# Kernel tuning notes

Hardware: AMD Instinct MI355X
Metric: run time of the kernel (lower is better)

Reference implementation:

```python
import jax, jax.numpy as jnp
import numpy as np

EPS = 1e-5

def layer_norm(x, w):
    mu = x.mean(-1, keepdims=True)
    var = x.var(-1, keepdims=True)
    return (x - mu) * jax.lax.rsqrt(var + EPS) * w

def multihead_norm(x, w):
    # x: (B,S,NH,DH) -> group norm per head, elementwise weight over NH*DH features
    mu = x.mean(-1, keepdims=True)
    var = x.var(-1, keepdims=True)
    xn = (x - mu) * jax.lax.rsqrt(var + EPS)
    B, S, NH, DH = x.shape
    return xn.reshape(B, S, NH * DH) * w

def causal_conv1d(x, W, b):
    # x: (B,S,C), W: (C,K) depthwise causal conv, bias b: (C,)
    C, K = W.shape
    ker = W.T[:, None, :]  # (K,1,C) in WIO layout
    y = jax.lax.conv_general_dilated(x, ker, (1,), [(K - 1, 0)],
                                     dimension_numbers=('NWC', 'WIO', 'NWC'),
                                     feature_group_count=C)
    return y + b

def headwise_linear(x, W):
    # block-diagonal linear; W: (nblocks, out, in)
    nb, o, i = W.shape
    B, S, F = x.shape
    y = jnp.einsum('bsni,noi->bsno', x.reshape(B, S, nb, i), W)
    return y.reshape(B, S, nb * o)

def mlstm_block(x, ln_w, up_W, conv_W, conv_b, q_W, k_W, v_W, ig_W, ig_b, fg_W, fg_b, on_w, skip, down_W):
    B, S, E = x.shape
    I = up_W.shape[1] // 2
    NH = ig_W.shape[0]
    DH = I // NH
    xn = layer_norm(x, ln_w)
    up = xn @ up_W                       # (B,S,2I)
    xm, z = up[..., :I], up[..., I:]
    xc = jax.nn.silu(causal_conv1d(xm, conv_W, conv_b))
    q = headwise_linear(xc, q_W)
    k = headwise_linear(xc, k_W)
    v = headwise_linear(xm, v_W)        # values come from the pre-conv branch
    gin = jnp.concatenate([q, k, v], -1)  # (B,S,3I)
    ig = (gin @ ig_W.T + ig_b).transpose(0, 2, 1)  # (B,NH,S)
    fg = (gin @ fg_W.T + fg_b).transpose(0, 2, 1)
    qh = q.reshape(B, S, NH, DH).transpose(0, 2, 1, 3)
    kh = k.reshape(B, S, NH, DH).transpose(0, 2, 1, 3)
    vh = v.reshape(B, S, NH, DH).transpose(0, 2, 1, 3)
    # parallel stabilized mLSTM (matrix memory)
    logf = jax.nn.log_sigmoid(fg)
    cs = jnp.concatenate([jnp.zeros_like(logf[..., :1]), jnp.cumsum(logf, -1)], -1)  # (B,NH,S+1)
    lf = cs[..., 1:, None] - cs[..., None, 1:]   # (B,NH,S,S): sum of log f over (t, s]
    mask = jnp.tril(jnp.ones((S, S), bool))
    log_D = jnp.where(mask, lf + ig[:, :, None, :], -jnp.inf)
    max_log_D = log_D.max(-1, keepdims=True)
    D = jnp.exp(log_D - max_log_D)
    qk = jnp.einsum('bhsd,bhtd->bhst', qh, kh) * (DH ** -0.5)
    C = qk * D
    normalizer = jnp.maximum(jnp.abs(C.sum(-1, keepdims=True)), jnp.exp(-max_log_D))
    h = jnp.einsum('bhst,bhtd->bhsd', C / (normalizer + 1e-6), vh)
    h = multihead_norm(h.transpose(0, 2, 1, 3), on_w)  # (B,S,I)
    h = (h + skip * xc) * jax.nn.silu(z)
    return x + h @ down_W

def slstm_block(x, ln_w, conv_W, conv_b, gates_W, R, bias, gn_w, ffn_ln_w, ffn_up_W, ffn_down_W):
    B, S, E = x.shape
    NH, DH = R.shape[0], R.shape[1]
    xn = layer_norm(x, ln_w)
    xc = jax.nn.silu(causal_conv1d(xn, conv_W, conv_b))
    xh = xn.reshape(B, S, NH, DH)
    xch = xc.reshape(B, S, NH, DH)
    i_pre = jnp.einsum('bsnd,nod->bsno', xch, gates_W[0])  # i,f gates see conv branch
    f_pre = jnp.einsum('bsnd,nod->bsno', xch, gates_W[1])
    z_pre = jnp.einsum('bsnd,nod->bsno', xh, gates_W[2])
    o_pre = jnp.einsum('bsnd,nod->bsno', xh, gates_W[3])
    gx = jnp.stack([i_pre, f_pre, z_pre, o_pre], 3) + bias  # (B,S,NH,4,DH)
    def step(carry, g):
        h, c, n, m = carry
        raw = g + jnp.einsum('bnd,ndg->bng', h, R).reshape(B, NH, 4, DH)
        ir, fr, zr, og = raw[:, :, 0], raw[:, :, 1], raw[:, :, 2], raw[:, :, 3]
        logfplusm = m + jax.nn.log_sigmoid(fr)
        m_new = jnp.maximum(ir, logfplusm)
        i = jnp.exp(ir - m_new)
        f = jnp.exp(logfplusm - m_new)
        c_new = f * c + i * jnp.tanh(zr)
        n_new = f * n + i
        h_new = jax.nn.sigmoid(og) * c_new / n_new
        return (h_new, c_new, n_new, m_new), h_new
    z0 = jnp.zeros((B, NH, DH), x.dtype)
    _, hs = jax.lax.scan(step, (z0, z0, z0, z0), gx.transpose(1, 0, 2, 3, 4))
    y = multihead_norm(hs.transpose(1, 0, 2, 3), gn_w)  # (B,S,E)
    x = x + y
    xn2 = layer_norm(x, ffn_ln_w)
    gpre, upp = jnp.split(xn2 @ ffn_up_W, 2, -1)
    return x + (jax.nn.gelu(gpre, approximate=False) * upp) @ ffn_down_W

def forward(x, m_ln_w, m_up_W, m_conv_W, m_conv_b, m_q_W, m_k_W, m_v_W, m_ig_W, m_ig_b, m_fg_W, m_fg_b, m_outnorm_w, m_skip, m_down_W, s_ln_w, s_conv_W, s_conv_b, s_gates_W, s_R, s_bias, s_gn_w, s_ffn_ln_w, s_ffn_up_W, s_ffn_down_W, post_norm_w, fc_W, fc_b):
    mi = 0
    for blk in range(7):  # slstm_at=[1]
        if blk == 1:
            x = slstm_block(x, s_ln_w, s_conv_W, s_conv_b, s_gates_W, s_R, s_bias, s_gn_w, s_ffn_ln_w, s_ffn_up_W, s_ffn_down_W)
        else:
            x = mlstm_block(x, m_ln_w[mi], m_up_W[mi], m_conv_W[mi], m_conv_b[mi], m_q_W[mi], m_k_W[mi], m_v_W[mi], m_ig_W[mi], m_ig_b[mi], m_fg_W[mi], m_fg_b[mi], m_outnorm_w[mi], m_skip[mi], m_down_W[mi])
            mi += 1
    x = layer_norm(x, post_norm_w)
    return x[:, -1, :] @ fc_W + fc_b

def setup_inputs():
    key = jax.random.key(0)
    ks = jax.random.split(key, 18)
    B, S, E = 16, 512, 128
    I, NH = 256, 4
    DHs = E // NH
    FF = 192
    NB = 6
    r = lambda k, shape, sc: jax.random.normal(k, shape, jnp.float32) * sc
    return dict(
        x=r(ks[0], (B, S, E), 1.0),
        m_ln_w=jnp.ones((NB, E), jnp.float32),
        m_up_W=r(ks[1], (NB, E, 2 * I), E ** -0.5),
        m_conv_W=r(ks[2], (NB, I, 4), 0.3),
        m_conv_b=jnp.zeros((NB, I), jnp.float32),
        m_q_W=r(ks[3], (NB, 64, 4, 4), 0.5),
        m_k_W=r(ks[4], (NB, 64, 4, 4), 0.5),
        m_v_W=r(ks[5], (NB, 64, 4, 4), 0.5),
        m_ig_W=r(ks[6], (NB, NH, 3 * I), 0.1 * (3 * I) ** -0.5),
        m_ig_b=r(ks[7], (NB, NH), 0.5),
        m_fg_W=r(ks[8], (NB, NH, 3 * I), 0.1 * (3 * I) ** -0.5),
        m_fg_b=r(ks[9], (NB, NH), 1.0) + 3.0,
        m_outnorm_w=jnp.ones((NB, I), jnp.float32),
        m_skip=jnp.ones((NB, I), jnp.float32),
        m_down_W=r(ks[10], (NB, I, E), I ** -0.5),
        s_ln_w=jnp.ones((E,), jnp.float32),
        s_conv_W=r(ks[11], (E, 4), 0.3),
        s_conv_b=jnp.zeros((E,), jnp.float32),
        s_gates_W=r(ks[12], (4, NH, DHs, DHs), DHs ** -0.5),
        s_R=r(ks[13], (NH, DHs, 4 * DHs), 0.5 * DHs ** -0.5),
        s_bias=r(ks[14], (NH, 4, DHs), 0.1),
        s_gn_w=jnp.ones((E,), jnp.float32),
        s_ffn_ln_w=jnp.ones((E,), jnp.float32),
        s_ffn_up_W=r(ks[15], (E, 2 * FF), E ** -0.5),
        s_ffn_down_W=r(ks[16], (FF, E), FF ** -0.5),
        post_norm_w=jnp.ones((E,), jnp.float32),
        fc_W=r(ks[17], (E, 1), E ** -0.5),
        fc_b=jnp.zeros((1,), jnp.float32),
    )

def reference(x, m_ln_w, m_up_W, m_conv_W, m_conv_b, m_q_W, m_k_W, m_v_W, m_ig_W, m_ig_b, m_fg_W, m_fg_b, m_outnorm_w, m_skip, m_down_W, s_ln_w, s_conv_W, s_conv_b, s_gates_W, s_R, s_bias, s_gn_w, s_ffn_ln_w, s_ffn_up_W, s_ffn_down_W, post_norm_w, fc_W, fc_b):
    return forward(x, m_ln_w, m_up_W, m_conv_W, m_conv_b, m_q_W, m_k_W, m_v_W, m_ig_W, m_ig_b, m_fg_W, m_fg_b, m_outnorm_w, m_skip, m_down_W, s_ln_w, s_conv_W, s_conv_b, s_gates_W, s_R, s_bias, s_gn_w, s_ffn_ln_w, s_ffn_up_W, s_ffn_down_W, post_norm_w, fc_W, fc_b)
```

## Files before the change

kernel.cpp:

```cpp
#include <hip/hip_runtime.h>
#include <cstddef>

constexpr int B = 16, S = 512, E = 128, I = 256, DHm = 64;
constexpr int BS = B * S;

typedef _Float16 half8 __attribute__((ext_vector_type(8)));
typedef _Float16 half4 __attribute__((ext_vector_type(4)));
typedef float f32x4 __attribute__((ext_vector_type(4)));

__device__ __forceinline__ int swz(int row, int col) {
  return (row * 64 + col) ^ ((row & 7) << 3);
}
struct h3s { _Float16 a, b, c; };
__device__ __forceinline__ h3s split3(float x) {
  h3s r;
  r.a = (_Float16)x;
  float t = x - (float)r.a;
  r.b = (_Float16)t;
  t -= (float)r.b;
  r.c = (_Float16)t;
  return r;
}
struct h2s { _Float16 a, b; };
__device__ __forceinline__ h2s split2(float x) {
  h2s r;
  r.a = (_Float16)x;
  r.b = (_Float16)(x - (float)r.a);
  return r;
}

template <int K, bool ADD, int FUSE>
__global__ void __launch_bounds__(256) gemm3(const float* __restrict__ A,
                                             const float* __restrict__ W,
                                             const float* __restrict__ lnw,
                                             float* __restrict__ C, int N, int astride) {
  __shared__ _Float16 A1[4096], A2[4096];
  __shared__ _Float16 B1[4096], B2[4096];
  __shared__ float smu[64], srr[64];
  const int n0 = blockIdx.x * 64, m0 = blockIdx.y * 64;
  const int tid = threadIdx.x;
  const int lane = tid & 63, w = tid >> 6;
  const int sband = w * 16;
  const int fr = lane & 15, fg = lane >> 4;

  if constexpr (FUSE == 1) {
    int row = tid >> 2, q = tid & 3;
    const float* ap = A + (size_t)(m0 + row) * astride + q * 32;
    float s1 = 0.f, s2 = 0.f;
#pragma unroll
    for (int i = 0; i < 8; i++) {
      float4 v = *(const float4*)(ap + i * 4);
      s1 += v.x + v.y + v.z + v.w;
      s2 += v.x * v.x + v.y * v.y + v.z * v.z + v.w * v.w;
    }
    s1 += __shfl_xor(s1, 1); s2 += __shfl_xor(s2, 1);
    s1 += __shfl_xor(s1, 2); s2 += __shfl_xor(s2, 2);
    if (q == 0) {
      float mu = s1 * (1.f / 128);
      float var = s2 * (1.f / 128) - mu * mu;
      smu[row] = mu;
      srr[row] = rsqrtf(var + 1e-5f);
    }
  }

  f32x4 acc[4] = {};
#pragma unroll
  for (int k0 = 0; k0 < K; k0 += 64) {
    __syncthreads();
#pragma unroll
    for (int i = 0; i < 4; i++) {
      int lin = tid + i * 256;
      int mm = lin >> 4, kq = (lin & 15) * 4;
      float4 a4;
      if constexpr (FUSE == 2) {
// ... 27 lines not shown
    }
#pragma unroll
    for (int i = 0; i < 4; i++) {
      int lin = tid + i * 256;
      int kk = lin >> 4, nq = (lin & 15) * 4;
      float4 w4 = *(const float4*)(W + (size_t)(k0 + kk) * N + n0 + nq);
      const float wv[4] = {w4.x, w4.y, w4.z, w4.w};
#pragma unroll
      for (int j = 0; j < 4; j++) {
        h2s sp = split2(wv[j]);
        B1[swz(nq + j, kk)] = sp.a;
        B2[swz(nq + j, kk)] = sp.b;
      }
    }
    __syncthreads();
    half8 a1g0 = *(const half8*)&A1[swz(sband + fr, fg * 8)];
    half8 a1g1 = *(const half8*)&A1[swz(sband + fr, 32 + fg * 8)];
    half8 a2g0 = *(const half8*)&A2[swz(sband + fr, fg * 8)];
    half8 a2g1 = *(const half8*)&A2[swz(sband + fr, 32 + fg * 8)];
#pragma unroll
    for (int ct = 0; ct < 4; ct++) {
      half8 b1g0 = *(const half8*)&B1[swz(ct * 16 + fr, fg * 8)];
      half8 b1g1 = *(const half8*)&B1[swz(ct * 16 + fr, 32 + fg * 8)];
      half8 b2g0 = *(const half8*)&B2[swz(ct * 16 + fr, fg * 8)];
      half8 b2g1 = *(const half8*)&B2[swz(ct * 16 + fr, 32 + fg * 8)];
      acc[ct] = __builtin_amdgcn_mfma_f32_16x16x32_f16(a2g0, b1g0, acc[ct], 0, 0, 0);
      acc[ct] = __builtin_amdgcn_mfma_f32_16x16x32_f16(a1g0, b2g0, acc[ct], 0, 0, 0);
      acc[ct] = __builtin_amdgcn_mfma_f32_16x16x32_f16(a1g0, b1g0, acc[ct], 0, 0, 0);
      acc[ct] = __builtin_amdgcn_mfma_f32_16x16x32_f16(a2g1, b1g1, acc[ct], 0, 0, 0);
      acc[ct] = __builtin_amdgcn_mfma_f32_16x16x32_f16(a1g1, b2g1, acc[ct], 0, 0, 0);
      acc[ct] = __builtin_amdgcn_mfma_f32_16x16x32_f16(a1g1, b1g1, acc[ct], 0, 0, 0);
    }
  }
#pragma unroll
  for (int ct = 0; ct < 4; ct++) {
#pragma unroll
    for (int r = 0; r < 4; r++) {
      int row = m0 + sband + fg * 4 + r;
      int col = n0 + ct * 16 + fr;
      float v = acc[ct][r];
      if (ADD) v += C[(size_t)row * N + col];
      C[(size_t)row * N + col] = v;
    }
  }
}

__global__ void __launch_bounds__(256) mlstm_mid_kernel(
    const float* __restrict__ UP, const float* __restrict__ conv_W,
    const float* __restrict__ conv_b, const float* __restrict__ qW,
    const float* __restrict__ kW, const float* __restrict__ vW,
    const float* __restrict__ igW, const float* __restrict__ igb,
    const float* __restrict__ fgW, const float* __restrict__ fgb,
    float* __restrict__ XC, float* __restrict__ Q,
    _Float16* __restrict__ K1, _Float16* __restrict__ K2, _Float16* __restrict__ K3,
    _Float16* __restrict__ V1t, _Float16* __restrict__ V2t, _Float16* __restrict__ V3t,
    float* __restrict__ IG, float* __restrict__ FG) {
  __shared__ float xcl[I], xml[I], qkvl[768];
  __shared__ float red[32];
  int r = blockIdx.x, t = threadIdx.x;
  int s = r & (S - 1);
  const float* xr = UP + (size_t)r * 512 + t;
  float4 w4 = *(const float4*)(conv_W + t * 4);
  float x0 = xr[0];
  float acc = conv_b[t] + x0 * w4.w;
  if (s >= 1) acc += xr[-512] * w4.z;
  if (s >= 2) acc += xr[-1024] * w4.y;
  if (s >= 3) acc += xr[-1536] * w4.x;
  float xc = acc / (1.f + __expf(-acc));
  xcl[t] = xc;
  xml[t] = x0;
  XC[(size_t)r * I + t] = xc;
  __syncthreads();
  int n = t >> 2, o = t & 3;
  const float* qw = qW + n * 16 + o * 4;
  const float* kw = kW + n * 16 + o * 4;
  const float* vw = vW + n * 16 + o * 4;
  float q = 0, k = 0, v = 0;
#pragma unroll
  for (int i = 0; i < 4; i++) {
    float xcv = xcl[n * 4 + i], xmv = xml[n * 4 + i];
    q += xcv * qw[i]; k += xcv * kw[i]; v += xmv * vw[i];
  }
  Q[(size_t)r * I + t] = q;
  {
    h3s sp = split3(k);
    K1[(size_t)r * I + t] = sp.a;
    K2[(size_t)r * I + t] = sp.b;
    K3[(size_t)r * I + t] = sp.c;
  }
  {
    int b = r >> 9, srow = r & (S - 1);
    int h = t >> 6, d = t & 63;
    size_t idx = ((size_t)(b * 4 + h) * 64 + d) * S + srow;
    h3s sp = split3(v);
    V1t[idx] = sp.a;
    V2t[idx] = sp.b;
    V3t[idx] = sp.c;
  }
  qkvl[t] = q; qkvl[256 + t] = k; qkvl[512 + t] = v;
  __syncthreads();
  float ai[4] = {}, af[4] = {};
#pragma unroll
  for (int j = 0; j < 3; j++) {
    int c = t + j * 256;
    float g = qkvl[c];
#pragma unroll
    for (int h = 0; h < 4; h++) {
      ai[h] += g * igW[h * 768 + c];
      af[h] += g * fgW[h * 768 + c];
    }
  }
#pragma unroll
  for (int m = 32; m; m >>= 1)
#pragma unroll
    for (int h = 0; h < 4; h++) {
      ai[h] += __shfl_xor(ai[h], m);
      af[h] += __shfl_xor(af[h], m);
    }
  int wv = t >> 6;
  if ((t & 63) == 0) {
#pragma unroll
    for (int h = 0; h < 4; h++) { red[wv * 8 + h] = ai[h]; red[wv * 8 + 4 + h] = af[h]; }
  }
  __syncthreads();
  if (t < 8) {
    float sum = red[t] + red[8 + t] + red[16 + t] + red[24 + t];
    int b = r >> 9, srow = r & (S - 1);
    int h = t & 3;
    if (t < 4) IG[((size_t)(b * 4 + h)) * S + srow] = sum + igb[h];
    else FG[((size_t)(b * 4 + h)) * S + srow] = sum + fgb[h];
  }
}

__global__ void __launch_bounds__(256) attn_mfma_kernel(
    const float* __restrict__ Q,
    const _Float16* __restrict__ K1g, const _Float16* __restrict__ K2g,
    const _Float16* __restrict__ K3g, const _Float16* __restrict__ V1g,
    const _Float16* __restrict__ V2g, const _Float16* __restrict__ V3g,
    const float* __restrict__ IG, const float* __restrict__ FG,
    const float* __restrict__ XC, const float* __restrict__ UP,
    const float* __restrict__ onw, const float* __restrict__ skip,
    float* __restrict__ HF) {
  __shared__ _Float16 K1[4096], K2[4096], K3[4096];
  __shared__ _Float16 V1[4096], V2[4096], V3[4096];
  __shared__ _Float16 W1[4096], W2[4096], W3[4096];
  __shared__ float A_l[512], M_l[512], F_l[512];
  int bid = blockIdx.x;
  int st = bid & 7, bh = bid >> 3;
  int b = bh >> 2, h = bh & 3;
  int s0 = st * 64;
  int tid = threadIdx.x;
  const float* Qg = Q + ((size_t)b * S) * I + h * DHm;
  const _Float16* K1p = K1g + ((size_t)b * S) * I + h * DHm;
  const _Float16* K2p = K2g + ((size_t)b * S) * I + h * DHm;
  const _Float16* K3p = K3g + ((size_t)b * S) * I + h * DHm;
  const _Float16* V1p = V1g + (size_t)bh * 64 * S;
  const _Float16* V2p = V2g + (size_t)bh * 64 * S;
  const _Float16* V3p = V3g + (size_t)bh * 64 * S;

  const int lane = tid & 63, w = tid >> 6;
  const int sband = w * 16;
  const int fr = lane & 15, fg = lane >> 4;

  if (tid < 64) {
    int l = tid;
    const float* ig = IG + (size_t)bh * S;
    const float* fgp = FG + (size_t)bh * S;
    float lfc[8], av[8], amx[8];
    float cs = 0;
#pragma unroll
    for (int j = 0; j < 8; j++) {
      float f = fgp[l * 8 + j];
      cs += fminf(f, 0.f) - log1pf(__expf(-fabsf(f)));
      lfc[j] = cs;
    }
    float tot = cs, inc = tot;
#pragma unroll
    for (int off = 1; off < 64; off <<= 1) {
      float yv = __shfl_up(inc, off);
      if (l >= off) inc += yv;
    }
    float excl = inc - tot;
    float pm = -1e30f;
#pragma unroll
    for (int j = 0; j < 8; j++) {
      float CSj = excl + lfc[j];
      av[j] = ig[l * 8 + j] - CSj;
      pm = fmaxf(pm, av[j]);
      amx[j] = pm;
      lfc[j] = CSj;
    }
    float incm = pm;
#pragma unroll
    for (int off = 1; off < 64; off <<= 1) {
      float yv = __shfl_up(incm, off);
      if (l >= off) incm = fmaxf(incm, yv);
    }
    float exclm = __shfl_up(incm, 1);
    if (l == 0) exclm = -1e30f;
#pragma unroll
    for (int j = 0; j < 8; j++) {
      float Mj = fmaxf(exclm, amx[j]);
      A_l[l * 8 + j] = av[j];
      M_l[l * 8 + j] = Mj;
      F_l[l * 8 + j] = __expf(-(lfc[j] + Mj));
    }
  }

  half8 aq1[2], aq2[2], aq3[2];
  {
    const float* qrow = Qg + (size_t)(s0 + sband + fr) * I;
#pragma unroll
    for (int c = 0; c < 2; c++) {
      float4 qa = *(const float4*)(qrow + c * 32 + fg * 8);
      float4 qb = *(const float4*)(qrow + c * 32 + fg * 8 + 4);
      float qv[8] = {qa.x, qa.y, qa.z, qa.w, qb.x, qb.y, qb.z, qb.w};
#pragma unroll
      for (int j = 0; j < 8; j++) {
        h3s sp = split3(qv[j]);
        aq1[c][j] = sp.a; aq2[c][j] = sp.b; aq3[c][j] = sp.c;
      }
    }
  }
  __syncthreads();
  float msl[4];
#pragma unroll
  for (int r = 0; r < 4; r++) msl[r] = M_l[s0 + sband + fg * 4 + r];

  f32x4 hacc[4] = {};
  float csp[4] = {};

  for (int tt = 0; tt <= st; tt++) {
    int t0 = tt * 64;
    __syncthreads();
#pragma unroll
    for (int i = 0; i < 4; i++) {
      int lin = tid + i * 256;
      int a = lin >> 4, q4 = (lin & 15) * 4;
      size_t koff = (size_t)(t0 + a) * I + q4;
      *(half4*)&K1[swz(a, q4)] = *(const half4*)(K1p + koff);
      *(half4*)&K2[swz(a, q4)] = *(const half4*)(K2p + koff);
      *(half4*)&K3[swz(a, q4)] = *(const half4*)(K3p + koff);
      size_t voff = (size_t)a * S + t0 + q4;
      *(half4*)&V1[swz(a, q4)] = *(const half4*)(V1p + voff);
      *(half4*)&V2[swz(a, q4)] = *(const half4*)(V2p + voff);
      *(half4*)&V3[swz(a, q4)] = *(const half4*)(V3p + voff);
    }
    __syncthreads();
#pragma unroll
    for (int ct = 0; ct < 4; ct++) {
      f32x4 sacc = {};
#pragma unroll
      for (int c = 0; c < 2; c++) {
        half8 b1 = *(const half8*)&K1[swz(ct * 16 + fr, c * 32 + fg * 8)];
        half8 b2 = *(const half8*)&K2[swz(ct * 16 + fr, c * 32 + fg * 8)];
        half8 b3 = *(const half8*)&K3[swz(ct * 16 + fr, c * 32 + fg * 8)];
        sacc = __builtin_amdgcn_mfma_f32_16x16x32_f16(aq3[c], b1, sacc, 0, 0, 0);
        sacc = __builtin_amdgcn_mfma_f32_16x16x32_f16(aq2[c], b2, sacc, 0, 0, 0);
        sacc = __builtin_amdgcn_mfma_f32_16x16x32_f16(aq1[c], b3, sacc, 0, 0, 0);
        sacc = __builtin_amdgcn_mfma_f32_16x16x32_f16(aq2[c], b1, sacc, 0, 0, 0);
        sacc = __builtin_amdgcn_mfma_f32_16x16x32_f16(aq1[c], b2, sacc, 0, 0, 0);
        sacc = __builtin_amdgcn_mfma_f32_16x16x32_f16(aq1[c], b1, sacc, 0, 0, 0);
      }
      int tg = t0 + ct * 16 + fr;
      float ea = A_l[tg];
#pragma unroll
      for (int r = 0; r < 4; r++) {
        int sl = sband + fg * 4 + r;
        float wv = 0.f;
        if (tg <= s0 + sl) wv = sacc[r] * 0.125f * __expf(ea - msl[r]);
        csp[r] += wv;
        h3s sp = split3(wv);
        W1[swz(sl, ct * 16 + fr)] = sp.a;
        W2[swz(sl, ct * 16 + fr)] = sp.b;
        W3[swz(sl, ct * 16 + fr)] = sp.c;
      }
    }
#pragma unroll
    for (int kc = 0; kc < 2; kc++) {
      half8 w1 = *(const half8*)&W1[swz(sband + fr, kc * 32 + fg * 8)];
      half8 w2 = *(const half8*)&W2[swz(sband + fr, kc * 32 + fg * 8)];
      half8 w3 = *(const half8*)&W3[swz(sband + fr, kc * 32 + fg * 8)];
#pragma unroll
      for (int dt = 0; dt < 4; dt++) {
        half8 v1 = *(const half8*)&V1[swz(dt * 16 + fr, kc * 32 + fg * 8)];
        half8 v2 = *(const half8*)&V2[swz(dt * 16 + fr, kc * 32 + fg * 8)];
        half8 v3 = *(const half8*)&V3[swz(dt * 16 + fr, kc * 32 + fg * 8)];
        hacc[dt] = __builtin_amdgcn_mfma_f32_16x16x32_f16(w3, v1, hacc[dt], 0, 0, 0);
        hacc[dt] = __builtin_amdgcn_mfma_f32_16x16x32_f16(w2, v2, hacc[dt], 0, 0, 0);
        hacc[dt] = __builtin_amdgcn_mfma_f32_16x16x32_f16(w1, v3, hacc[dt], 0, 0, 0);
        hacc[dt] = __builtin_amdgcn_mfma_f32_16x16x32_f16(w2, v1, hacc[dt], 0, 0, 0);
        hacc[dt] = __builtin_amdgcn_mfma_f32_16x16x32_f16(w1, v2, hacc[dt], 0, 0, 0);
        hacc[dt] = __builtin_amdgcn_mfma_f32_16x16x32_f16(w1, v1, hacc[dt], 0, 0, 0);
      }
    }
  }
#pragma unroll
  for (int m = 1; m < 16; m <<= 1)
#pragma unroll
    for (int r = 0; r < 4; r++) csp[r] += __shfl_xor(csp[r], m);
  float on4[4], sk4[4];
#pragma unroll
  for (int dt = 0; dt < 4; dt++) {
    on4[dt] = onw[h * DHm + dt * 16 + fr];
    sk4[dt] = skip[h * DHm + dt * 16 + fr];
  }
#pragma unroll
  for (int r = 0; r < 4; r++) {
    int sl = sband + fg * 4 + r;
    size_t row = (size_t)b * S + s0 + sl;
    float Fv = F_l[s0 + sl];
    float inv = 1.f / (fmaxf(fabsf(csp[r]), Fv) + 1e-6f);
    float hv[4], s1 = 0.f, s2 = 0.f;
#pragma unroll
    for (int dt = 0; dt < 4; dt++) {
      hv[dt] = hacc[dt][r] * inv;
      s1 += hv[dt];
      s2 += hv[dt] * hv[dt];
    }
#pragma unroll
    for (int m = 1; m < 16; m <<= 1) { s1 += __shfl_xor(s1, m); s2 += __shfl_xor(s2, m); }
    float mu = s1 * (1.f / 64), var = s2 * (1.f / 64) - mu * mu;
    float rr = rsqrtf(var + 1e-5f);
#pragma unroll
    for (int dt = 0; dt < 4; dt++) {
      int col = h * DHm + dt * 16 + fr;
      float xc = XC[row * I + col];
      float zv = UP[row * (2 * I) + I + col];
      float hn = (hv[dt] - mu) * rr * on4[dt];
      HF[row * I + col] = (hn + sk4[dt] * xc) * (zv / (1.f + __expf(-zv)));
    }
  }
}

__global__ void __launch_bounds__(512) slstm_pre_kernel(
    const float* __restrict__ X, const float* __restrict__ lnw,
    const float* __restrict__ conv_W, const float* __restrict__ conv_b,
    const float* __restrict__ gW, const float* __restrict__ bias,
    float* __restrict__ GX) {
  __shared__ float xnl[4][128], xcl[128];
  __shared__ float redS[8], redQ[8];
  int r = blockIdx.x, t = threadIdx.x;
  int s = r & (S - 1);
  int b0 = r - s;
  int rr = t >> 7, cc = t & 127;
  int sr = s - 3 + rr;
  int grow = b0 + (sr > 0 ? sr : 0);
  float x = X[(size_t)grow * E + cc];
  float s1 = x, s2 = x * x;
#pragma unroll
  for (int m = 32; m; m >>= 1) { s1 += __shfl_xor(s1, m); s2 += __shfl_xor(s2, m); }
  int wv = t >> 6;
  if ((t & 63) == 0) { redS[wv] = s1; redQ[wv] = s2; }
  __syncthreads();
  float fs1 = redS[rr * 2] + redS[rr * 2 + 1];
  float fs2 = redQ[rr * 2] + redQ[rr * 2 + 1];
  float mu = fs1 * (1.f / 128);
  float var = fs2 * (1.f / 128) - mu * mu;
  xnl[rr][cc] = (x - mu) * rsqrtf(var + 1e-5f) * lnw[cc];
  __syncthreads();
  if (t < 128) {
    float4 w4 = *(const float4*)(conv_W + t * 4);
    float acc = conv_b[t] + xnl[3][t] * w4.w;
    if (s >= 1) acc += xnl[2][t] * w4.z;
    if (s >= 2) acc += xnl[1][t] * w4.y;
    if (s >= 3) acc += xnl[0][t] * w4.x;
    xcl[t] = acc / (1.f + __expf(-acc));
  }
  __syncthreads();
  int n = t >> 7, g = (t >> 5) & 3, o = t & 31;
  const float* src = (g < 2) ? (xcl + n * 32) : (xnl[3] + n * 32);
  const float* wp = gW + (((size_t)g * 4 + n) * 32 + o) * 32;
  float acc = bias[n * 128 + g * 32 + o];
#pragma unroll
  for (int d = 0; d < 32; d++) acc += src[d] * wp[d];
  GX[(size_t)r * 512 + t] = acc;
}

__global__ void __launch_bounds__(128) slstm_scan8(const float* __restrict__ GX,
                                                   const float* __restrict__ R,
                                                   float* __restrict__ HS) {
  constexpr int CH = 16, NCH = S / CH;
  __shared__ float ring[2][CH][128];
  int blk = blockIdx.x;
  int b = blk >> 2, n = blk & 3;
  int tid = threadIdx.x;
  int wv = tid >> 6, l = tid & 63;
  const float* gxp = GX + ((size_t)b * S) * 512 + n * 128;

  float R0[32], R1[32];
  float h_own = 0.f, c = 0.f, nn = 0.f, m = 0.f;
  if (wv == 0) {
#pragma unroll
    for (int d = 0; d < 32; d++) {
      R0[d] = R[((size_t)(n * 32 + d)) * 128 + l];
      R1[d] = R[((size_t)(n * 32 + d)) * 128 + 64 + l];
    }
  } else {
    float v0[CH], v1[CH];
#pragma unroll
    for (int j = 0; j < CH; j++) {
      v0[j] = gxp[(size_t)j * 512 + l];
      v1[j] = gxp[(size_t)j * 512 + 64 + l];
    }
#pragma unroll
    for (int j = 0; j < CH; j++) {
      ring[0][j][l] = v0[j];
      ring[0][j][64 + l] = v1[j];
    }
  }
  __syncthreads();

  for (int ck = 0; ck < NCH; ck++) {
    if (wv == 1) {
      if (ck + 1 < NCH) {
        const float* src = gxp + (size_t)(ck + 1) * CH * 512;
        float v0[CH], v1[CH];
#pragma unroll
        for (int j = 0; j < CH; j++) {
          v0[j] = src[(size_t)j * 512 + l];
          v1[j] = src[(size_t)j * 512 + 64 + l];
        }
        int pb = (ck + 1) & 1;
#pragma unroll
        for (int j = 0; j < CH; j++) {
          ring[pb][j][l] = v0[j];
          ring[pb][j][64 + l] = v1[j];
        }
      }
    } else {
      int cb = ck & 1;
#pragma unroll
      for (int j = 0; j < CH; j++) {
        float g0 = ring[cb][j][l];
        float g1 = ring[cb][j][64 + l];
        float r0p0 = g0, r0p1 = 0.f, r0p2 = 0.f, r0p3 = 0.f;
        float r1p0 = g1, r1p1 = 0.f, r1p2 = 0.f, r1p3 = 0.f;
#pragma unroll
        for (int d = 0; d < 32; d += 4) {
          float hv0 = __shfl(h_own, d);
          float hv1 = __shfl(h_own, d + 1);
          float hv2 = __shfl(h_own, d + 2);
          float hv3 = __shfl(h_own, d + 3);
          r0p0 += hv0 * R0[d];     r1p0 += hv0 * R1[d];
          r0p1 += hv1 * R0[d + 1]; r1p1 += hv1 * R1[d + 1];
          r0p2 += hv2 * R0[d + 2]; r1p2 += hv2 * R1[d + 2];
          r0p3 += hv3 * R0[d + 3]; r1p3 += hv3 * R1[d + 3];
        }
        float raw0 = (r0p0 + r0p1) + (r0p2 + r0p3);
        float raw1 = (r1p0 + r1p1) + (r1p2 + r1p3);
        float fr = __shfl_down(raw0, 32);
        float og = __shfl_down(raw1, 32);
        float ir = raw0, zr = raw1;
        float lsf = fminf(fr, 0.f) - __logf(1.f + __expf(-fabsf(fr)));
        float lfm = m + lsf;
        float mn = fmaxf(ir, lfm);
        float iv = __expf(ir - mn), fv = __expf(lfm - mn);
        float th = 1.f - 2.f / (__expf(2.f * zr) + 1.f);
        c = fv * c + iv * th;
        nn = fv * nn + iv;
        m = mn;
        float hv = (c / nn) / (1.f + __expf(-og));
        h_own = hv;
        int s = ck * CH + j;
        if (l < 32) HS[((size_t)(b * S + s)) * E + n * 32 + l] = hv;
      }
    }
    __syncthreads();
  }
}

__global__ void gnorm_add_kernel(const float* __restrict__ HS, const float* __restrict__ gnw,
                                 float* __restrict__ X) {
  int r = blockIdx.x, t = threadIdx.x;
  float v = HS[(size_t)r * E + t];
  float s1 = v, s2 = v * v;
#pragma unroll
  for (int m = 16; m; m >>= 1) { s1 += __shfl_xor(s1, m, 32); s2 += __shfl_xor(s2, m, 32); }
  float mu = s1 * (1.f / 32), var = s2 * (1.f / 32) - mu * mu;
  X[(size_t)r * E + t] += (v - mu) * rsqrtf(var + 1e-5f) * gnw[t];
}

__global__ void head_kernel(const float* __restrict__ X, const float* __restrict__ pw,
                            const float* __restrict__ fcW, const float* __restrict__ fcb,
                            float* __restrict__ out) {
  int b = blockIdx.x, l = threadIdx.x;
  const float* xr = X + ((size_t)(b * S + S - 1)) * E;
  float2 v = *(const float2*)(xr + l * 2);
  float s1 = v.x + v.y, s2 = v.x * v.x + v.y * v.y;
#pragma unroll
  for (int m = 32; m; m >>= 1) { s1 += __shfl_xor(s1, m); s2 += __shfl_xor(s2, m); }
  float mu = s1 * (1.f / E), var = s2 * (1.f / E) - mu * mu;
  float rr = rsqrtf(var + 1e-5f);
  float2 wv = *(const float2*)(pw + l * 2);
  float2 fw = *(const float2*)(fcW + l * 2);
  float acc = (v.x - mu) * rr * wv.x * fw.x + (v.y - mu) * rr * wv.y * fw.y;
#pragma unroll
  for (int m = 32; m; m >>= 1) acc += __shfl_xor(acc, m);
  if (l == 0) out[b] = acc + fcb[0];
}

extern "C" void kernel_launch(void* const* d_in, const int* in_sizes, int n_in, void* d_out,
                              int out_size, void* d_ws, size_t ws_size, hipStream_t stream) {
  const float* in_x = (const float*)d_in[0];
  const float* m_ln_w = (const float*)d_in[1];
  const float* m_up_W = (const float*)d_in[2];
  const float* m_conv_W = (const float*)d_in[3];
  const float* m_conv_b = (const float*)d_in[4];
  const float* m_q_W = (const float*)d_in[5];
  const float* m_k_W = (const float*)d_in[6];
  const float* m_v_W = (const float*)d_in[7];
  const float* m_ig_W = (const float*)d_in[8];
  const float* m_ig_b = (const float*)d_in[9];
  const float* m_fg_W = (const float*)d_in[10];
  const float* m_fg_b = (const float*)d_in[11];
  const float* m_on_w = (const float*)d_in[12];
  const float* m_skip = (const float*)d_in[13];
  const float* m_down_W = (const float*)d_in[14];
  const float* s_ln_w = (const float*)d_in[15];
  const float* s_conv_W = (const float*)d_in[16];
  const float* s_conv_b = (const float*)d_in[17];
  const float* s_gates_W = (const float*)d_in[18];
  const float* s_R = (const float*)d_in[19];
  const float* s_bias = (const float*)d_in[20];
  const float* s_gn_w = (const float*)d_in[21];
  const float* s_ffn_ln_w = (const float*)d_in[22];
  const float* s_ffn_up_W = (const float*)d_in[23];
  const float* s_ffn_down_W = (const float*)d_in[24];
  const float* post_norm_w = (const float*)d_in[25];
  const float* fc_W = (const float*)d_in[26];
  const float* fc_b = (const float*)d_in[27];

  float* ws = (float*)d_ws;
  float* X = ws;
  float* UP = X + 1048576;
  float* XC = UP + 4194304;
  float* Qb = XC + 2097152;
  float* Hb = Qb + 2097152;
  float* IGb = Hb + 2097152;
  float* FGb = IGb + 32768;
  _Float16* F16 = (_Float16*)(FGb + 32768);
  _Float16* K1 = F16;
  _Float16* K2 = K1 + 2097152;
  _Float16* K3 = K2 + 2097152;
  _Float16* V1t = K3 + 2097152;
  _Float16* V2t = V1t + 2097152;
  _Float16* V3t = V2t + 2097152;

  hipMemcpyAsync(X, in_x, (size_t)BS * E * sizeof(float), hipMemcpyDeviceToDevice, stream);

  int mi = 0;
  for (int blk = 0; blk < 7; blk++) {
    if (blk == 1) {
      slstm_pre_kernel<<<BS, 512, 0, stream>>>(X, s_ln_w, s_conv_W, s_conv_b, s_gates_W,
                                               s_bias, UP);
      slstm_scan8<<<64, 128, 0, stream>>>(UP, s_R, Hb);
      gnorm_add_kernel<<<BS, E, 0, stream>>>(Hb, s_gn_w, X);
      gemm3<128, false, 1><<<dim3(6, 128), 256, 0, stream>>>(X, s_ffn_up_W, s_ffn_ln_w, UP,
                                                             384, 128);
      gemm3<192, true, 2><<<dim3(2, 128), 256, 0, stream>>>(UP, s_ffn_down_W, nullptr, X,
                                                            128, 384);
    } else {
      const float* ln_w = m_ln_w + (size_t)mi * E;
      const float* up_W = m_up_W + (size_t)mi * E * 512;
      const float* conv_W = m_conv_W + (size_t)mi * I * 4;
      const float* conv_b = m_conv_b + (size_t)mi * I;
      const float* q_W = m_q_W + (size_t)mi * 1024;
      const float* k_W = m_k_W + (size_t)mi * 1024;
      const float* v_W = m_v_W + (size_t)mi * 1024;
      const float* ig_W = m_ig_W + (size_t)mi * 3072;
      const float* ig_b = m_ig_b + (size_t)mi * 4;
      const float* fg_W = m_fg_W + (size_t)mi * 3072;
      const float* fg_b = m_fg_b + (size_t)mi * 4;
      const float* on_w = m_on_w + (size_t)mi * I;
      const float* skipv = m_skip + (size_t)mi * I;
      const float* down_W = m_down_W + (size_t)mi * I * E;

      gemm3<128, false, 1><<<dim3(8, 128), 256, 0, stream>>>(X, up_W, ln_w, UP, 512, 128);
      mlstm_mid_kernel<<<BS, 256, 0, stream>>>(UP, conv_W, conv_b, q_W, k_W, v_W, ig_W, ig_b,
                                               fg_W, fg_b, XC, Qb, K1, K2, K3, V1t, V2t, V3t,
                                               IGb, FGb);
      attn_mfma_kernel<<<512, 256, 0, stream>>>(Qb, K1, K2, K3, V1t, V2t, V3t, IGb, FGb, XC,
                                                UP, on_w, skipv, Hb);
      gemm3<256, true, 0><<<dim3(2, 128), 256, 0, stream>>>(Hb, down_W, nullptr, X, 128, 256);
      mi++;
    }
  }
  head_kernel<<<B, 64, 0, stream>>>(X, post_norm_w, fc_W, fc_b, (float*)d_out);
}
```

Baseline: 1.279 ms.

## Pair causal query tiles per block to balance work and share K/V loads

Each attention block now handles two query tiles, a long one (7-st4) and a short one (st4), so every block runs the same number of key/value tile iterations under the causal mask. The grid shrinks from 512 to 256 blocks. K/V tiles staged in shared memory are reused by both query tiles, which removes duplicate global loads. In exchange each block holds twice as many accumulators and Q fragments, which raises register pressure and may lower occupancy.

Measured after the change: 1.311 ms. 2.6% more time.

```diff
diff --git a/kernel.cpp b/kernel.cpp
--- a/kernel.cpp
+++ b/kernel.cpp
@@ -247,9 +247,10 @@
   __shared__ _Float16 W1[4096], W2[4096], W3[4096];
   __shared__ float A_l[512], M_l[512], F_l[512];
   int bid = blockIdx.x;
-  int st = bid & 7, bh = bid >> 3;
+  int st4 = bid & 3, bh = bid >> 2;
   int b = bh >> 2, h = bh & 3;
-  int s0 = st * 64;
+  const int stA = 7 - st4, stB = st4;
+  const int s0A = stA * 64, s0B = stB * 64;
   int tid = threadIdx.x;
   const float* Qg = Q + ((size_t)b * S) * I + h * DHm;
   const _Float16* K1p = K1g + ((size_t)b * S) * I + h * DHm;
@@ -308,30 +309,42 @@
     }
   }
 
-  half8 aq1[2], aq2[2], aq3[2];
+  half8 aq1A[2], aq2A[2], aq3A[2], aq1B[2], aq2B[2], aq3B[2];
   {
-    const float* qrow = Qg + (size_t)(s0 + sband + fr) * I;
+    const float* qrowA = Qg + (size_t)(s0A + sband + fr) * I;
+    const float* qrowB = Qg + (size_t)(s0B + sband + fr) * I;
 #pragma unroll
     for (int c = 0; c < 2; c++) {
-      float4 qa = *(const float4*)(qrow + c * 32 + fg * 8);
-      float4 qb = *(const float4*)(qrow + c * 32 + fg * 8 + 4);
+      float4 qa = *(const float4*)(qrowA + c * 32 + fg * 8);
+      float4 qb = *(const float4*)(qrowA + c * 32 + fg * 8 + 4);
       float qv[8] = {qa.x, qa.y, qa.z, qa.w, qb.x, qb.y, qb.z, qb.w};
 #pragma unroll
       for (int j = 0; j < 8; j++) {
         h3s sp = split3(qv[j]);
-        aq1[c][j] = sp.a; aq2[c][j] = sp.b; aq3[c][j] = sp.c;
+        aq1A[c][j] = sp.a; aq2A[c][j] = sp.b; aq3A[c][j] = sp.c;
+      }
+      float4 qc = *(const float4*)(qrowB + c * 32 + fg * 8);
+      float4 qd = *(const float4*)(qrowB + c * 32 + fg * 8 + 4);
+      float qw[8] = {qc.x, qc.y, qc.z, qc.w, qd.x, qd.y, qd.z, qd.w};
+#pragma unroll
+      for (int j = 0; j < 8; j++) {
+        h3s sp = split3(qw[j]);
+        aq1B[c][j] = sp.a; aq2B[c][j] = sp.b; aq3B[c][j] = sp.c;
       }
     }
   }
   __syncthreads();
-  float msl[4];
-#pragma unroll
-  for (int r = 0; r < 4; r++) msl[r] = M_l[s0 + sband + fg * 4 + r];
-
-  f32x4 hacc[4] = {};
-  float csp[4] = {};
-
-  for (int tt = 0; tt <= st; tt++) {
+  float mslA[4], mslB[4];
+#pragma unroll
+  for (int r = 0; r < 4; r++) {
+    mslA[r] = M_l[s0A + sband + fg * 4 + r];
+    mslB[r] = M_l[s0B + sband + fg * 4 + r];
+  }
+
+  f32x4 haccA[4] = {}, haccB[4] = {};
+  float cspA[4] = {}, cspB[4] = {};
+
+  for (int tt = 0; tt <= stA; tt++) {
     int t0 = tt * 64;
     __syncthreads();
 #pragma unroll
@@ -356,12 +369,15 @@
         half8 b1 = *(const half8*)&K1[swz(ct * 16 + fr, c * 32 + fg * 8)];
         half8 b2 = *(const half8*)&K2[swz(ct * 16 + fr, c * 32 + fg * 8)];
         half8 b3 = *(const half8*)&K3[swz(ct * 16 + fr, c * 32 + fg * 8)];
-        sacc = __builtin_amdgcn_mfma_f32_16x16x32_f16(aq3[c], b1, sacc, 0, 0, 0);
-        sacc = __builtin_amdgcn_mfma_f32_16x16x32_f16(aq2[c], b2, sacc, 0, 0, 0);
-        sacc = __builtin_amdgcn_mfma_f32_16x16x32_f16(aq1[c], b3, sacc, 0, 0, 0);
-        sacc = __builtin_amdgcn_mfma_f32_16x16x32_f16(aq2[c], b1, sacc, 0, 0, 0);
-        sacc = __builtin_amdgcn_mfma_f32_16x16x32_f16(aq1[c], b2, sacc, 0, 0, 0);
-        sacc = __builtin_amdgcn_mfma_f32_16x16x32_f16(aq1[c], b1, sacc, 0, 0, 0);
+        half8 a1 = c ? aq1A[1] : aq1A[0];
+        half8 a2 = c ? aq2A[1] : aq2A[0];
+        half8 a3 = c ? aq3A[1] : aq3A[0];
+        sacc = __builtin_amdgcn_mfma_f32_16x16x32_f16(a3, b1, sacc, 0, 0, 0);
+        sacc = __builtin_amdgcn_mfma_f32_16x16x32_f16(a2, b2, sacc, 0, 0, 0);
+        sacc = __builtin_amdgcn_mfma_f32_16x16x32_f16(a1, b3, sacc, 0, 0, 0);
+        sacc = __builtin_amdgcn_mfma_f32_16x16x32_f16(a2, b1, sacc, 0, 0, 0);
+        sacc = __builtin_amdgcn_mfma_f32_16x16x32_f16(a1, b2, sacc, 0, 0, 0);
+        sacc = __builtin_amdgcn_mfma_f32_16x16x32_f16(a1, b1, sacc, 0, 0, 0);
       }
       int tg = t0 + ct * 16 + fr;
       float ea = A_l[tg];
@@ -369,8 +385,8 @@
       for (int r = 0; r < 4; r++) {
         int sl = sband + fg * 4 + r;
         float wv = 0.f;
-        if (tg <= s0 + sl) wv = sacc[r] * 0.125f * __expf(ea - msl[r]);
-        csp[r] += wv;
+        if (tg <= s0A + sl) wv = sacc[r] * 0.125f * __expf(ea - mslA[r]);
+        cspA[r] += wv;
         h3s sp = split3(wv);
         W1[swz(sl, ct * 16 + fr)] = sp.a;
         W2[swz(sl, ct * 16 + fr)] = sp.b;
@@ -387,19 +403,74 @@
         half8 v1 = *(const half8*)&V1[swz(dt * 16 + fr, kc * 32 + fg * 8)];
         half8 v2 = *(const half8*)&V2[swz(dt * 16 + fr, kc * 32 + fg * 8)];
         half8 v3 = *(const half8*)&V3[swz(dt * 16 + fr, kc * 32 + fg * 8)];
-        hacc[dt] = __builtin_amdgcn_mfma_f32_16x16x32_f16(w3, v1, hacc[dt], 0, 0, 0);
-        hacc[dt] = __builtin_amdgcn_mfma_f32_16x16x32_f16(w2, v2, hacc[dt], 0, 0, 0);
-        hacc[dt] = __builtin_amdgcn_mfma_f32_16x16x32_f16(w1, v3, hacc[dt], 0, 0, 0);
-        hacc[dt] = __builtin_amdgcn_mfma_f32_16x16x32_f16(w2, v1, hacc[dt], 0, 0, 0);
-        hacc[dt] = __builtin_amdgcn_mfma_f32_16x16x32_f16(w1, v2, hacc[dt], 0, 0, 0);
-        hacc[dt] = __builtin_amdgcn_mfma_f32_16x16x32_f16(w1, v1, hacc[dt], 0, 0, 0);
+        haccA[dt] = __builtin_amdgcn_mfma_f32_16x16x32_f16(w3, v1, haccA[dt], 0, 0, 0);
+        haccA[dt] = __builtin_amdgcn_mfma_f32_16x16x32_f16(w2, v2, haccA[dt], 0, 0, 0);
+        haccA[dt] = __builtin_amdgcn_mfma_f32_16x16x32_f16(w1, v3, haccA[dt], 0, 0, 0);
+        haccA[dt] = __builtin_amdgcn_mfma_f32_16x16x32_f16(w2, v1, haccA[dt], 0, 0, 0);
+        haccA[dt] = __builtin_amdgcn_mfma_f32_16x16x32_f16(w1, v2, haccA[dt], 0, 0, 0);
+        haccA[dt] = __builtin_amdgcn_mfma_f32_16x16x32_f16(w1, v1, haccA[dt], 0, 0, 0);
+      }
+    }
+    if (tt <= stB) {
+#pragma unroll
+      for (int ct = 0; ct < 4; ct++) {
+        f32x4 sacc = {};
+#pragma unroll
+        for (int c = 0; c < 2; c++) {
+          half8 b1 = *(const half8*)&K1[swz(ct * 16 + fr, c * 32 + fg * 8)];
+          half8 b2 = *(const half8*)&K2[swz(ct * 16 + fr, c * 32 + fg * 8)];
+          half8 b3 = *(const half8*)&K3[swz(ct * 16 + fr, c * 32 + fg * 8)];
+          half8 a1 = c ? aq1B[1] : aq1B[0];
+          half8 a2 = c ? aq2B[1] : aq2B[0];
+          half8 a3 = c ? aq3B[1] : aq3B[0];
+          sacc = __builtin_amdgcn_mfma_f32_16x16x32_f16(a3, b1, sacc, 0, 0, 0);
+          sacc = __builtin_amdgcn_mfma_f32_16x16x32_f16(a2, b2, sacc, 0, 0, 0);
+          sacc = __builtin_amdgcn_mfma_f32_16x16x32_f16(a1, b3, sacc, 0, 0, 0);
+          sacc = __builtin_amdgcn_mfma_f32_16x16x32_f16(a2, b1, sacc, 0, 0, 0);
+          sacc = __builtin_amdgcn_mfma_f32_16x16x32_f16(a1, b2, sacc, 0, 0, 0);
+          sacc = __builtin_amdgcn_mfma_f32_16x16x32_f16(a1, b1, sacc, 0, 0, 0);
+        }
+        int tg = t0 + ct * 16 + fr;
+        float ea = A_l[tg];
+#pragma unroll
+        for (int r = 0; r < 4; r++) {
+          int sl = sband + fg * 4 + r;
+          float wv = 0.f;
+          if (tg <= s0B + sl) wv = sacc[r] * 0.125f * __expf(ea - mslB[r]);
+          cspB[r] += wv;
+          h3s sp = split3(wv);
+          W1[swz(sl, ct * 16 + fr)] = sp.a;
+          W2[swz(sl, ct * 16 + fr)] = sp.b;
+          W3[swz(sl, ct * 16 + fr)] = sp.c;
+        }
+      }
+#pragma unroll
+      for (int kc = 0; kc < 2; kc++) {
+        half8 w1 = *(const half8*)&W1[swz(sband + fr, kc * 32 + fg * 8)];
+        half8 w2 = *(const half8*)&W2[swz(sband + fr, kc * 32 + fg * 8)];
+        half8 w3 = *(const half8*)&W3[swz(sband + fr, kc * 32 + fg * 8)];
+#pragma unroll
+        for (int dt = 0; dt < 4; dt++) {
+          half8 v1 = *(const half8*)&V1[swz(dt * 16 + fr, kc * 32 + fg * 8)];
+          half8 v2 = *(const half8*)&V2[swz(dt * 16 + fr, kc * 32 + fg * 8)];
+          half8 v3 = *(const half8*)&V3[swz(dt * 16 + fr, kc * 32 + fg * 8)];
+          haccB[dt] = __builtin_amdgcn_mfma_f32_16x16x32_f16(w3, v1, haccB[dt], 0, 0, 0);
+          haccB[dt] = __builtin_amdgcn_mfma_f32_16x16x32_f16(w2, v2, haccB[dt], 0, 0, 0);
+          haccB[dt] = __builtin_amdgcn_mfma_f32_16x16x32_f16(w1, v3, haccB[dt], 0, 0, 0);
+          haccB[dt] = __builtin_amdgcn_mfma_f32_16x16x32_f16(w2, v1, haccB[dt], 0, 0, 0);
+          haccB[dt] = __builtin_amdgcn_mfma_f32_16x16x32_f16(w1, v2, haccB[dt], 0, 0, 0);
+          haccB[dt] = __builtin_amdgcn_mfma_f32_16x16x32_f16(w1, v1, haccB[dt], 0, 0, 0);
+        }
       }
     }
   }
 #pragma unroll
   for (int m = 1; m < 16; m <<= 1)
 #pragma unroll
-    for (int r = 0; r < 4; r++) csp[r] += __shfl_xor(csp[r], m);
+    for (int r = 0; r < 4; r++) {
+      cspA[r] += __shfl_xor(cspA[r], m);
+      cspB[r] += __shfl_xor(cspB[r], m);
+    }
   float on4[4], sk4[4];
 #pragma unroll
   for (int dt = 0; dt < 4; dt++) {
@@ -407,29 +478,34 @@
     sk4[dt] = skip[h * DHm + dt * 16 + fr];
   }
 #pragma unroll
-  for (int r = 0; r < 4; r++) {
-    int sl = sband + fg * 4 + r;
-    size_t row = (size_t)b * S + s0 + sl;
-    float Fv = F_l[s0 + sl];
-    float inv = 1.f / (fmaxf(fabsf(csp[r]), Fv) + 1e-6f);
-    float hv[4], s1 = 0.f, s2 = 0.f;
-#pragma unroll
-    for (int dt = 0; dt < 4; dt++) {
-      hv[dt] = hacc[dt][r] * inv;
-      s1 += hv[dt];
-      s2 += hv[dt] * hv[dt];
-    }
-#pragma unroll
-    for (int m = 1; m < 16; m <<= 1) { s1 += __shfl_xor(s1, m); s2 += __shfl_xor(s2, m); }
-    float mu = s1 * (1.f / 64), var = s2 * (1.f / 64) - mu * mu;
-    float rr = rsqrtf(var + 1e-5f);
-#pragma unroll
-    for (int dt = 0; dt < 4; dt++) {
-      int col = h * DHm + dt * 16 + fr;
-      float xc = XC[row * I + col];
-      float zv = UP[row * (2 * I) + I + col];
-      float hn = (hv[dt] - mu) * rr * on4[dt];
-      HF[row * I + col] = (hn + sk4[dt] * xc) * (zv / (1.f + __expf(-zv)));
+  for (int part = 0; part < 2; part++) {
+    int s0p = part ? s0B : s0A;
+#pragma unroll
+    for (int r = 0; r < 4; r++) {
+      int sl = sband + fg * 4 + r;
+      size_t row = (size_t)b * S + s0p + sl;
+      float Fv = F_l[s0p + sl];
+      float cspv = part ? cspB[r] : cspA[r];
+      float inv = 1.f / (fmaxf(fabsf(cspv), Fv) + 1e-6f);
+      float hv[4], s1 = 0.f, s2 = 0.f;
+#pragma unroll
+      for (int dt = 0; dt < 4; dt++) {
+        hv[dt] = (part ? haccB[dt][r] : haccA[dt][r]) * inv;
+        s1 += hv[dt];
+        s2 += hv[dt] * hv[dt];
+      }
+#pragma unroll
+      for (int m = 1; m < 16; m <<= 1) { s1 += __shfl_xor(s1, m); s2 += __shfl_xor(s2, m); }
+      float mu = s1 * (1.f / 64), var = s2 * (1.f / 64) - mu * mu;
+      float rr = rsqrtf(var + 1e-5f);
+#pragma unroll
+      for (int dt = 0; dt < 4; dt++) {
+        int col = h * DHm + dt * 16 + fr;
+        float xc = XC[row * I + col];
+        float zv = UP[row * (2 * I) + I + col];
+        float hn = (hv[dt] - mu) * rr * on4[dt];
+        HF[row * I + col] = (hn + sk4[dt] * xc) * (zv / (1.f + __expf(-zv)));
+      }
     }
   }
 }
@@ -681,7 +757,7 @@
       mlstm_mid_kernel<<<BS, 256, 0, stream>>>(UP, conv_W, conv_b, q_W, k_W, v_W, ig_W, ig_b,
                                                fg_W, fg_b, XC, Qb, K1, K2, K3, V1t, V2t, V3t,
                                                IGb, FGb);
-      attn_mfma_kernel<<<512, 256, 0, stream>>>(Qb, K1, K2, K3, V1t, V2t, V3t, IGb, FGb, XC,
+      attn_mfma_kernel<<<256, 256, 0, stream>>>(Qb, K1, K2, K3, V1t, V2t, V3t, IGb, FGb, XC,
                                                 UP, on_w, skipv, Hb);
       gemm3<256, true, 0><<<dim3(2, 128), 256, 0, stream>>>(Hb, down_W, nullptr, X, 128, 256);
       mi++;
```

## Use two-term fp16 splits in mLSTM attention and fuse sLSTM groupnorm into scan

Applied to the files above, without the earlier changes.

The mLSTM attention used to emulate fp32 matmuls with a three-way fp16 split and six MFMAs per product. It now uses a two-way split with three MFMAs, which removes the K3/V3/W3 buffers, their global and LDS traffic, and half the MFMA work. The sLSTM per-head group norm and residual add are also folded into the scan kernel, so one launch and the HS round trip go away. The lower-precision split risks accuracy loss in the attention products.

Measured after the change: 1.098 ms. -14.1%, faster.

```diff
diff --git a/kernel.cpp b/kernel.cpp
--- a/kernel.cpp
+++ b/kernel.cpp
@@ -10,16 +10,6 @@
 
 __device__ __forceinline__ int swz(int row, int col) {
   return (row * 64 + col) ^ ((row & 7) << 3);
-}
-struct h3s { _Float16 a, b, c; };
-__device__ __forceinline__ h3s split3(float x) {
-  h3s r;
-  r.a = (_Float16)x;
-  float t = x - (float)r.a;
-  r.b = (_Float16)t;
-  t -= (float)r.b;
-  r.c = (_Float16)t;
-  return r;
 }
 struct h2s { _Float16 a, b; };
 __device__ __forceinline__ h2s split2(float x) {
@@ -153,8 +143,8 @@
     const float* __restrict__ igW, const float* __restrict__ igb,
     const float* __restrict__ fgW, const float* __restrict__ fgb,
     float* __restrict__ XC, float* __restrict__ Q,
-    _Float16* __restrict__ K1, _Float16* __restrict__ K2, _Float16* __restrict__ K3,
-    _Float16* __restrict__ V1t, _Float16* __restrict__ V2t, _Float16* __restrict__ V3t,
+    _Float16* __restrict__ K1, _Float16* __restrict__ K2,
+    _Float16* __restrict__ V1t, _Float16* __restrict__ V2t,
     float* __restrict__ IG, float* __restrict__ FG) {
   __shared__ float xcl[I], xml[I], qkvl[768];
   __shared__ float red[32];
@@ -184,19 +174,17 @@
   }
   Q[(size_t)r * I + t] = q;
   {
-    h3s sp = split3(k);
+    h2s sp = split2(k);
     K1[(size_t)r * I + t] = sp.a;
     K2[(size_t)r * I + t] = sp.b;
-    K3[(size_t)r * I + t] = sp.c;
   }
   {
     int b = r >> 9, srow = r & (S - 1);
     int h = t >> 6, d = t & 63;
     size_t idx = ((size_t)(b * 4 + h) * 64 + d) * S + srow;
-    h3s sp = split3(v);
+    h2s sp = split2(v);
     V1t[idx] = sp.a;
     V2t[idx] = sp.b;
-    V3t[idx] = sp.c;
   }
   qkvl[t] = q; qkvl[256 + t] = k; qkvl[512 + t] = v;
   __syncthreads();
@@ -236,15 +224,14 @@
 __global__ void __launch_bounds__(256) attn_mfma_kernel(
     const float* __restrict__ Q,
     const _Float16* __restrict__ K1g, const _Float16* __restrict__ K2g,
-    const _Float16* __restrict__ K3g, const _Float16* __restrict__ V1g,
-    const _Float16* __restrict__ V2g, const _Float16* __restrict__ V3g,
+    const _Float16* __restrict__ V1g, const _Float16* __restrict__ V2g,
     const float* __restrict__ IG, const float* __restrict__ FG,
     const float* __restrict__ XC, const float* __restrict__ UP,
     const float* __restrict__ onw, const float* __restrict__ skip,
     float* __restrict__ HF) {
-  __shared__ _Float16 K1[4096], K2[4096], K3[4096];
-  __shared__ _Float16 V1[4096], V2[4096], V3[4096];
-  __shared__ _Float16 W1[4096], W2[4096], W3[4096];
+  __shared__ _Float16 K1[4096], K2[4096];
+  __shared__ _Float16 V1[4096], V2[4096];
+  __shared__ _Float16 W1[4096], W2[4096];
   __shared__ float A_l[512], M_l[512], F_l[512];
   int bid = blockIdx.x;
   int st = bid & 7, bh = bid >> 3;
@@ -254,10 +241,8 @@
   const float* Qg = Q + ((size_t)b * S) * I + h * DHm;
   const _Float16* K1p = K1g + ((size_t)b * S) * I + h * DHm;
   const _Float16* K2p = K2g + ((size_t)b * S) * I + h * DHm;
-  const _Float16* K3p = K3g + ((size_t)b * S) * I + h * DHm;
   const _Float16* V1p = V1g + (size_t)bh * 64 * S;
   const _Float16* V2p = V2g + (size_t)bh * 64 * S;
-  const _Float16* V3p = V3g + (size_t)bh * 64 * S;
 
   const int lane = tid & 63, w = tid >> 6;
   const int sband = w * 16;
@@ -308,7 +293,7 @@
     }
   }
 
-  half8 aq1[2], aq2[2], aq3[2];
+  half8 aq1[2], aq2[2];
   {
     const float* qrow = Qg + (size_t)(s0 + sband + fr) * I;
 #pragma unroll
@@ -318,8 +303,8 @@
       float qv[8] = {qa.x, qa.y, qa.z, qa.w, qb.x, qb.y, qb.z, qb.w};
 #pragma unroll
       for (int j = 0; j < 8; j++) {
-        h3s sp = split3(qv[j]);
-        aq1[c][j] = sp.a; aq2[c][j] = sp.b; aq3[c][j] = sp.c;
+        h2s sp = split2(qv[j]);
+        aq1[c][j] = sp.a; aq2[c][j] = sp.b;
       }
     }
   }
@@ -341,11 +326,9 @@
       size_t koff = (size_t)(t0 + a) * I + q4;
       *(half4*)&K1[swz(a, q4)] = *(const half4*)(K1p + koff);
       *(half4*)&K2[swz(a, q4)] = *(const half4*)(K2p + koff);
-      *(half4*)&K3[swz(a, q4)] = *(const half4*)(K3p + koff);
       size_t voff = (size_t)a * S + t0 + q4;
       *(half4*)&V1[swz(a, q4)] = *(const half4*)(V1p + voff);
       *(half4*)&V2[swz(a, q4)] = *(const half4*)(V2p + voff);
-      *(half4*)&V3[swz(a, q4)] = *(const half4*)(V3p + voff);
     }
     __syncthreads();
 #pragma unroll
@@ -355,10 +338,6 @@
       for (int c = 0; c < 2; c++) {
         half8 b1 = *(const half8*)&K1[swz(ct * 16 + fr, c * 32 + fg * 8)];
         half8 b2 = *(const half8*)&K2[swz(ct * 16 + fr, c * 32 + fg * 8)];
-        half8 b3 = *(const half8*)&K3[swz(ct * 16 + fr, c * 32 + fg * 8)];
-        sacc = __builtin_amdgcn_mfma_f32_16x16x32_f16(aq3[c], b1, sacc, 0, 0, 0);
-        sacc = __builtin_amdgcn_mfma_f32_16x16x32_f16(aq2[c], b2, sacc, 0, 0, 0);
-        sacc = __builtin_amdgcn_mfma_f32_16x16x32_f16(aq1[c], b3, sacc, 0, 0, 0);
         sacc = __builtin_amdgcn_mfma_f32_16x16x32_f16(aq2[c], b1, sacc, 0, 0, 0);
         sacc = __builtin_amdgcn_mfma_f32_16x16x32_f16(aq1[c], b2, sacc, 0, 0, 0);
         sacc = __builtin_amdgcn_mfma_f32_16x16x32_f16(aq1[c], b1, sacc, 0, 0, 0);
@@ -371,25 +350,19 @@
         float wv = 0.f;
         if (tg <= s0 + sl) wv = sacc[r] * 0.125f * __expf(ea - msl[r]);
         csp[r] += wv;
-        h3s sp = split3(wv);
+        h2s sp = split2(wv);
         W1[swz(sl, ct * 16 + fr)] = sp.a;
         W2[swz(sl, ct * 16 + fr)] = sp.b;
-        W3[swz(sl, ct * 16 + fr)] = sp.c;
       }
     }
 #pragma unroll
     for (int kc = 0; kc < 2; kc++) {
       half8 w1 = *(const half8*)&W1[swz(sband + fr, kc * 32 + fg * 8)];
       half8 w2 = *(const half8*)&W2[swz(sband + fr, kc * 32 + fg * 8)];
-      half8 w3 = *(const half8*)&W3[swz(sband + fr, kc * 32 + fg * 8)];
 #pragma unroll
       for (int dt = 0; dt < 4; dt++) {
         half8 v1 = *(const half8*)&V1[swz(dt * 16 + fr, kc * 32 + fg * 8)];
         half8 v2 = *(const half8*)&V2[swz(dt * 16 + fr, kc * 32 + fg * 8)];
-        half8 v3 = *(const half8*)&V3[swz(dt * 16 + fr, kc * 32 + fg * 8)];
-        hacc[dt] = __builtin_amdgcn_mfma_f32_16x16x32_f16(w3, v1, hacc[dt], 0, 0, 0);
-        hacc[dt] = __builtin_amdgcn_mfma_f32_16x16x32_f16(w2, v2, hacc[dt], 0, 0, 0);
-        hacc[dt] = __builtin_amdgcn_mfma_f32_16x16x32_f16(w1, v3, hacc[dt], 0, 0, 0);
         hacc[dt] = __builtin_amdgcn_mfma_f32_16x16x32_f16(w2, v1, hacc[dt], 0, 0, 0);
         hacc[dt] = __builtin_amdgcn_mfma_f32_16x16x32_f16(w1, v2, hacc[dt], 0, 0, 0);
         hacc[dt] = __builtin_amdgcn_mfma_f32_16x16x32_f16(w1, v1, hacc[dt], 0, 0, 0);
@@ -478,9 +451,10 @@
   GX[(size_t)r * 512 + t] = acc;
 }
 
-__global__ void __launch_bounds__(128) slstm_scan8(const float* __restrict__ GX,
+__global__ void __launch_bounds__(128) slstm_scan9(const float* __restrict__ GX,
                                                    const float* __restrict__ R,
-                                                   float* __restrict__ HS) {
+                                                   const float* __restrict__ gnw,
+                                                   float* __restrict__ X) {
   constexpr int CH = 16, NCH = S / CH;
   __shared__ float ring[2][CH][128];
   int blk = blockIdx.x;
@@ -491,12 +465,14 @@
 
   float R0[32], R1[32];
   float h_own = 0.f, c = 0.f, nn = 0.f, m = 0.f;
+  float gnl = 0.f;
   if (wv == 0) {
 #pragma unroll
     for (int d = 0; d < 32; d++) {
       R0[d] = R[((size_t)(n * 32 + d)) * 128 + l];
       R1[d] = R[((size_t)(n * 32 + d)) * 128 + 64 + l];
     }
+    if (l < 32) gnl = gnw[n * 32 + l];
   } else {
     float v0[CH], v1[CH];
 #pragma unroll
@@ -563,23 +539,20 @@
         m = mn;
         float hv = (c / nn) / (1.f + __expf(-og));
         h_own = hv;
+        float s1 = hv, s2 = hv * hv;
+#pragma unroll
+        for (int mm2 = 16; mm2; mm2 >>= 1) {
+          s1 += __shfl_xor(s1, mm2, 32);
+          s2 += __shfl_xor(s2, mm2, 32);
+        }
+        float mu = s1 * (1.f / 32), var = s2 * (1.f / 32) - mu * mu;
+        float hn = (hv - mu) * rsqrtf(var + 1e-5f) * gnl;
         int s = ck * CH + j;
-        if (l < 32) HS[((size_t)(b * S + s)) * E + n * 32 + l] = hv;
+        if (l < 32) X[((size_t)(b * S + s)) * E + n * 32 + l] += hn;
       }
     }
     __syncthreads();
   }
-}
-
-__global__ void gnorm_add_kernel(const float* __restrict__ HS, const float* __restrict__ gnw,
-                                 float* __restrict__ X) {
-  int r = blockIdx.x, t = threadIdx.x;
-  float v = HS[(size_t)r * E + t];
-  float s1 = v, s2 = v * v;
-#pragma unroll
-  for (int m = 16; m; m >>= 1) { s1 += __shfl_xor(s1, m, 32); s2 += __shfl_xor(s2, m, 32); }
-  float mu = s1 * (1.f / 32), var = s2 * (1.f / 32) - mu * mu;
-  X[(size_t)r * E + t] += (v - mu) * rsqrtf(var + 1e-5f) * gnw[t];
 }
 
 __global__ void head_kernel(const float* __restrict__ X, const float* __restrict__ pw,
@@ -643,10 +616,8 @@
   _Float16* F16 = (_Float16*)(FGb + 32768);
   _Float16* K1 = F16;
   _Float16* K2 = K1 + 2097152;
-  _Float16* K3 = K2 + 2097152;
-  _Float16* V1t = K3 + 2097152;
+  _Float16* V1t = K2 + 2097152;
   _Float16* V2t = V1t + 2097152;
-  _Float16* V3t = V2t + 2097152;
 
   hipMemcpyAsync(X, in_x, (size_t)BS * E * sizeof(float), hipMemcpyDeviceToDevice, stream);
 
@@ -655,8 +626,7 @@
     if (blk == 1) {
       slstm_pre_kernel<<<BS, 512, 0, stream>>>(X, s_ln_w, s_conv_W, s_conv_b, s_gates_W,
                                                s_bias, UP);
-      slstm_scan8<<<64, 128, 0, stream>>>(UP, s_R, Hb);
-      gnorm_add_kernel<<<BS, E, 0, stream>>>(Hb, s_gn_w, X);
+      slstm_scan9<<<64, 128, 0, stream>>>(UP, s_R, s_gn_w, X);
       gemm3<128, false, 1><<<dim3(6, 128), 256, 0, stream>>>(X, s_ffn_up_W, s_ffn_ln_w, UP,
                                                              384, 128);
       gemm3<192, true, 2><<<dim3(2, 128), 256, 0, stream>>>(UP, s_ffn_down_W, nullptr, X,
@@ -679,10 +649,10 @@
 
       gemm3<128, false, 1><<<dim3(8, 128), 256, 0, stream>>>(X, up_W, ln_w, UP, 512, 128);
       mlstm_mid_kernel<<<BS, 256, 0, stream>>>(UP, conv_W, conv_b, q_W, k_W, v_W, ig_W, ig_b,
-                                               fg_W, fg_b, XC, Qb, K1, K2, K3, V1t, V2t, V3t,
-                                               IGb, FGb);
-      attn_mfma_kernel<<<512, 256, 0, stream>>>(Qb, K1, K2, K3, V1t, V2t, V3t, IGb, FGb, XC,
-                                                UP, on_w, skipv, Hb);
+                                               fg_W, fg_b, XC, Qb, K1, K2, V1t, V2t, IGb,
+                                               FGb);
+      attn_mfma_kernel<<<512, 256, 0, stream>>>(Qb, K1, K2, V1t, V2t, IGb, FGb, XC, UP, on_w,
+                                                skipv, Hb);
       gemm3<256, true, 0><<<dim3(2, 128), 256, 0, stream>>>(Hb, down_W, nullptr, X, 128, 256);
       mi++;
     }
```
